# Kernel optimization log

Measured on AMD Instinct MI355X. Metric: run time of the kernel, lower is better.

## Reference

```python
import jax, jax.numpy as jnp
import numpy as np
from jax import lax

B, N, HID = 2, 1024, 2048
H, D, HKV = 32, 64, 8
GROUPS = H // HKV
CHUNK = 64
MAG = 0.5
GATE_NORM = 16.0


def setup_inputs() -> dict:
    key = jax.random.key(0)
    ks = jax.random.split(key, 5)
    hidden_states = jax.random.normal(ks[0], (B, N, HID), jnp.float32)
    Wq = jax.random.normal(ks[1], (HID, H * D), jnp.float32) * 0.02
    Wk = jax.random.normal(ks[2], (HID, HKV * D), jnp.float32) * 0.02
    Wv = jax.random.normal(ks[3], (HID, HKV * D), jnp.float32) * 0.02
    Wo = jax.random.normal(ks[4], (H * D, HID), jnp.float32) * 0.02
    return {"hidden_states": hidden_states, "Wq": Wq, "Wk": Wk, "Wv": Wv, "Wo": Wo}


def _repeat_kv(x, g):
    # [b, hkv, n, d] -> [b, hkv*g, n, d]
    return jnp.repeat(x, g, axis=1)


def _delta_rule_chunked(q, k, v, beta, chunk):
    """Chunked delta-rule linear attention (DeltaNet-style) with elementwise beta gate."""
    b, h, n, d = q.shape
    nc = n // chunk
    qc, kc, vc, bc = (x.reshape(b, h, nc, chunk, d) for x in (q, k, v, beta))
    k_beta = kc * bc
    v_beta = vc * bc
    # T = (I + tril(k_beta k^T, -1))^{-1}, a unit lower-triangular solve per chunk
    strict = jnp.tril(jnp.ones((chunk, chunk), bool), -1)
    L = jnp.einsum('bhnid,bhnjd->bhnij', k_beta, kc) * strict
    M = L + jnp.eye(chunk, dtype=q.dtype)
    eye = jnp.broadcast_to(jnp.eye(chunk, dtype=q.dtype), M.shape)
    T = jax.scipy.linalg.solve_triangular(M, eye, lower=True, unit_diagonal=True)
    u = jnp.einsum('bhnij,bhnjd->bhnid', T, v_beta)   # pseudo-values
    w = jnp.einsum('bhnij,bhnjd->bhnid', T, k_beta)   # pseudo-keys
    causal = jnp.tril(jnp.ones((chunk, chunk), bool))

    def step(S, xs):
        qi, ki, ui, wi = xs  # each [b, h, chunk, d]; S: [b, h, d, d]
        u_p = ui - jnp.einsum('bhcd,bhde->bhce', wi, S)
        attn = jnp.einsum('bhid,bhjd->bhij', qi, ki) * causal
        o = jnp.einsum('bhcd,bhde->bhce', qi, S) + jnp.einsum('bhij,bhjd->bhid', attn, u_p)
        S_new = S + jnp.einsum('bhcd,bhce->bhde', ki, u_p)
        return S_new, o

    xs = tuple(jnp.moveaxis(x, 2, 0) for x in (qc, kc, u, w))  # [nc, b, h, chunk, d]
    S0 = jnp.zeros((b, h, d, d), q.dtype)
    S_final, o = lax.scan(step, S0, xs)
    o = jnp.moveaxis(o, 0, 2).reshape(b, h, n, d)
    return o, S_final


def reference(hidden_states, Wq, Wk, Wv, Wo):
    b, n, _ = hidden_states.shape
    q = hidden_states @ Wq            # [b, n, H*D]
    k = hidden_states @ Wk            # [b, n, HKV*D]
    v = hidden_states @ Wv            # [b, n, HKV*D]
    g = k  # AdaptiveAvgPool1d(512 -> 512) is the identity here

    qh = q.reshape(b, n, H, D).transpose(0, 2, 1, 3)      # [b, H, n, D]
    kh = k.reshape(b, n, HKV, D).transpose(0, 2, 1, 3)    # [b, HKV, n, D]
    vh = v.reshape(b, n, HKV, D).transpose(0, 2, 1, 3)
    gh = g.reshape(b, n, HKV, D).transpose(0, 2, 1, 3)
    k_rep = _repeat_kv(kh, GROUPS)
    v_rep = _repeat_kv(vh, GROUPS)
    g_rep = _repeat_kv(gh, GROUPS)

    # linear-attention branch: softmax feature maps + log-sigmoid gate
    ql = jax.nn.softmax(qh, axis=-1).astype(jnp.float32)
    kl = jax.nn.softmax(k_rep, axis=-1).astype(jnp.float32)
    gl = (jax.nn.log_sigmoid(g_rep) / GATE_NORM).astype(jnp.float32)
    o_lin, _ = _delta_rule_chunked(ql, kl, v_rep.astype(jnp.float32), gl, CHUNK)
    o_lin = o_lin.transpose(0, 2, 1, 3).reshape(b, n, H * D) @ Wo

    # base (vanilla causal) attention branch
    scale = 1.0 / np.sqrt(D).astype(np.float32)
    scores = jnp.einsum('bhid,bhjd->bhij', qh, k_rep) * scale
    causal = jnp.tril(jnp.ones((n, n), bool))
    scores = jnp.where(causal, scores, jnp.finfo(scores.dtype).min)
    attn_weights = jax.nn.softmax(scores, axis=-1)
    o_base = jnp.einsum('bhij,bhjd->bhid', attn_weights, v_rep)
    o_base = o_base.transpose(0, 2, 1, 3).reshape(b, n, H * D) @ Wo

    out = MAG * o_lin + (1.0 - MAG) * o_base
    return out, attn_weights
```

## Files before the change

kernel.cpp:

```cpp
#include <hip/hip_runtime.h>
#include <hip/hip_bf16.h>

constexpr int Bc = 2, Nc = 1024, HIDc = 2048, Hc = 32, Dc = 64, HKVc = 8, NCc = 16;

typedef unsigned short bfu;
typedef __attribute__((ext_vector_type(8))) short frag_ab;
typedef __attribute__((ext_vector_type(4))) float frag_cd;

__device__ __forceinline__ bfu f2bf(float f) {
  unsigned int u = __float_as_uint(f);
  unsigned int r = u + 0x7fffu + ((u >> 16) & 1u);
  return (bfu)(r >> 16);
}
__device__ __forceinline__ ushort4 pack4(float4 v) {
  ushort4 r; r.x = f2bf(v.x); r.y = f2bf(v.y); r.z = f2bf(v.z); r.w = f2bf(v.w);
  return r;
}

__device__ __forceinline__ void gl16(const bfu* g, bfu* l) {
  __builtin_amdgcn_global_load_lds(
      (const __attribute__((address_space(1))) void*)g,
      (__attribute__((address_space(3))) void*)l, 16, 0, 0);
}

__global__ __launch_bounds__(256) void cast_bf16_k(
    const float* __restrict__ in, bfu* __restrict__ out)
{
  const size_t i = ((size_t)blockIdx.x * 256 + threadIdx.x) * 4;
  *(ushort4*)(out + i) = pack4(*(const float4*)(in + i));
}

__global__ __launch_bounds__(256) void transpose_cast_k(
    const float* __restrict__ W, bfu* __restrict__ WT, int K, int N)
{
  __shared__ float t[32][33];
  const int bn = blockIdx.x * 32, bk = blockIdx.y * 32;
  const int x = threadIdx.x & 31, y = threadIdx.x >> 5;
#pragma unroll
  for (int i = 0; i < 32; i += 8)
    t[y + i][x] = W[(size_t)(bk + y + i) * N + bn + x];
  __syncthreads();
#pragma unroll
  for (int i = 0; i < 32; i += 8)
    WT[(size_t)(bn + y + i) * K + bk + x] = f2bf(t[x][y + i]);
}

__global__ __launch_bounds__(256) void transpose_v_k(
    const float* __restrict__ v, bfu* __restrict__ vt)
{
  __shared__ __align__(16) bfu T[64][72];
  const int blk = blockIdx.x;
  const int nt = blk & 15, bh = blk >> 4;
  const int hk = bh & 7, b = bh >> 3;
  const int tid = threadIdx.x;
  const int n = tid >> 2, dv0 = (tid & 3) * 16;
  const float* src = v + ((size_t)(b * Nc + nt * 64 + n) * 8 + hk) * 64 + dv0;
#pragma unroll
  for (int e = 0; e < 16; ++e) T[dv0 + e][n] = f2bf(src[e]);
  __syncthreads();
  const int r = tid >> 3, c = (tid & 7) * 8;
#pragma unroll
  for (int hh = 0; hh < 2; ++hh) {
    const int dv = r + hh * 32;
    *(uint4*)(vt + ((size_t)(bh * 64 + dv)) * 1024 + nt * 64 + c) =
        *(const uint4*)&T[dv][c];
  }
}

__device__ __forceinline__ void gemm128_gl(
    const bfu* __restrict__ A, const bfu* __restrict__ BT,
    float* __restrict__ C, const int Nn, const int m0, const int n0,
    bfu* As, bfu* Bs)
{
  const int tid = threadIdx.x;
  const int wave = tid >> 6, lane = tid & 63;
  const int wm = (wave >> 1) * 64, wn = (wave & 1) * 64;
  const int fm = lane & 15, quad = lane >> 4;
  const int sr = tid >> 2, skc = (tid & 3) * 8;

  frag_cd acc[4][4];
#pragma unroll
  for (int i = 0; i < 4; ++i)
#pragma unroll
    for (int j = 0; j < 4; ++j) acc[i][j] = (frag_cd){0.f, 0.f, 0.f, 0.f};

  const bfu* Ag = A + (size_t)(m0 + sr) * 2048 + skc;
  const bfu* Bg = BT + (size_t)(n0 + sr) * 2048 + skc;
  bfu* Al = As + tid * 8;
  bfu* Bl = Bs + tid * 8;

  for (int k0 = 0; k0 < 2048; k0 += 32) {
    gl16(Ag + k0, Al);
    gl16(Ag + k0 + (size_t)64 * 2048, Al + 64 * 32);
    gl16(Bg + k0, Bl);
    gl16(Bg + k0 + (size_t)64 * 2048, Bl + 64 * 32);
    __syncthreads();
    frag_ab a[4], b[4];
#pragma unroll
    for (int im = 0; im < 4; ++im)
      a[im] = *(const frag_ab*)&As[(size_t)(wm + im * 16 + fm) * 32 + quad * 8];
#pragma unroll
    for (int in = 0; in < 4; ++in)
      b[in] = *(const frag_ab*)&Bs[(size_t)(wn + in * 16 + fm) * 32 + quad * 8];
#pragma unroll
    for (int im = 0; im < 4; ++im)
#pragma unroll
      for (int in = 0; in < 4; ++in)
        acc[im][in] = __builtin_amdgcn_mfma_f32_16x16x32_bf16(
            a[im], b[in], acc[im][in], 0, 0, 0);
    __syncthreads();
  }
#pragma unroll
  for (int im = 0; im < 4; ++im)
#pragma unroll
    for (int in = 0; in < 4; ++in) {
      const int n = n0 + wn + in * 16 + fm;
#pragma unroll
      for (int r = 0; r < 4; ++r) {
        const int m = m0 + wm + im * 16 + quad * 4 + r;
        C[(size_t)m * Nn + n] = acc[im][in][r];
      }
    }
}

__global__ __launch_bounds__(256) void gemm_qkv_k(
    const bfu* __restrict__ A, const bfu* __restrict__ BTq,
    const bfu* __restrict__ BTk, const bfu* __restrict__ BTv,
    float* __restrict__ Cq, float* __restrict__ Ck, float* __restrict__ Cv)
{
  __shared__ __align__(16) bfu As[128 * 32];
  __shared__ __align__(16) bfu Bs[128 * 32];
  int bx = blockIdx.x;
  const bfu* BT; float* C; int Nn;
  if (bx < 16)      { BT = BTq; C = Cq; Nn = 2048; }
  else if (bx < 20) { BT = BTk; C = Ck; Nn = 512; bx -= 16; }
  else              { BT = BTv; C = Cv; Nn = 512; bx -= 20; }
  gemm128_gl(A, BT, C, Nn, blockIdx.y * 128, bx * 128, As, Bs);
}

__global__ __launch_bounds__(256) void gemm_wo_k(
    const bfu* __restrict__ A, const bfu* __restrict__ BT, float* __restrict__ C)
{
  __shared__ __align__(16) bfu As[128 * 32];
  __shared__ __align__(16) bfu Bs[128 * 32];
  gemm128_gl(A, BT, C, 2048, blockIdx.y * 128, blockIdx.x * 128, As, Bs);
}

__global__ __launch_bounds__(256) void gates64_k(
    const float* __restrict__ kin, float* __restrict__ kl, float* __restrict__ gl,
    bfu* __restrict__ k_bf)
{
  const int r = blockIdx.x * 4 + (threadIdx.x >> 6);
  const int lane = threadIdx.x & 63;
  const size_t idx = (size_t)r * 64 + lane;
  const float x = kin[idx];
  k_bf[idx] = f2bf(x);
  float m = x;
#pragma unroll
  for (int o = 32; o > 0; o >>= 1) m = fmaxf(m, __shfl_xor(m, o, 64));
  const float e = __expf(x - m);
  float s = e;
#pragma unroll
  for (int o = 32; o > 0; o >>= 1) s += __shfl_xor(s, o, 64);
  kl[idx] = e / s;
  const float ls = fminf(x, 0.f) - log1pf(__expf(-fabsf(x)));
  gl[idx] = ls * 0.0625f;
}

__global__ __launch_bounds__(256) void chunk_prep_k(
    const float* __restrict__ kl, const float* __restrict__ v,
    const float* __restrict__ gl, float* __restrict__ u_out, float* __restrict__ w_out)
{
  __shared__ __align__(16) float KC[64][68];
  __shared__ float KB[64][65];
  __shared__ float VB[64][65];
  const int blk = blockIdx.x;
  const int c = blk & 15, bh = blk >> 4;
  const int hk = bh & 7, b = bh >> 3;
  const int tid = threadIdx.x;
  for (int x = tid; x < 4096; x += 256) {
    const int i = x >> 6, d = x & 63;
    const size_t src = ((size_t)(b * Nc + c * 64 + i) * 8 + hk) * 64 + d;
    const float kv = kl[src], g = gl[src], vv = v[src];
    KC[d][i] = kv; KB[i][d] = kv * g; VB[i][d] = vv * g;
  }
  __syncthreads();
  const int li = tid >> 2, j0 = (tid & 3) * 16;
  float acc[16];
#pragma unroll
  for (int jj = 0; jj < 16; ++jj) acc[jj] = 0.f;
  for (int d = 0; d < 64; ++d) {
    const float kb = KB[li][d];
    const float4 c0v = *(const float4*)&KC[d][j0];
    const float4 c1v = *(const float4*)&KC[d][j0 + 4];
    const float4 c2v = *(const float4*)&KC[d][j0 + 8];
    const float4 c3v = *(const float4*)&KC[d][j0 + 12];
    acc[0] += kb * c0v.x;  acc[1] += kb * c0v.y;  acc[2] += kb * c0v.z;  acc[3] += kb * c0v.w;
    acc[4] += kb * c1v.x;  acc[5] += kb * c1v.y;  acc[6] += kb * c1v.z;  acc[7] += kb * c1v.w;
    acc[8] += kb * c2v.x;  acc[9] += kb * c2v.y;  acc[10] += kb * c2v.z; acc[11] += kb * c2v.w;
    acc[12] += kb * c3v.x; acc[13] += kb * c3v.y; acc[14] += kb * c3v.z; acc[15] += kb * c3v.w;
  }
  __syncthreads();
#pragma unroll
  for (int jj = 0; jj < 16; ++jj)
    KC[li][j0 + jj] = (j0 + jj < li) ? acc[jj] : 0.f;
  __syncthreads();
  for (int r0 = 0; r0 < 64; r0 += 16) {
    if (r0 > 0) {
      for (int p = tid; p < 2048; p += 256) {
        const int ii = p >> 7, dc = p & 127;
        float (*X)[65] = (dc < 64) ? VB : KB;
        const int d = dc & 63;
        float a2 = X[r0 + ii][d];
        for (int j = 0; j < r0; ++j) a2 -= KC[r0 + ii][j] * X[j][d];
        X[r0 + ii][d] = a2;
      }
      __syncthreads();
    }
    if (tid < 128) {
      const int d = tid & 63;
      float (*X)[65] = (tid < 64) ? VB : KB;
      for (int i = r0 + 1; i < r0 + 16; ++i) {
        float a2 = X[i][d];
        for (int j = r0; j < i; ++j) a2 -= KC[i][j] * X[j][d];
        X[i][d] = a2;
      }
    }
    __syncthreads();
  }
  for (int x = tid; x < 4096; x += 256) {
    u_out[(size_t)blk * 4096 + x] = VB[x >> 6][x & 63];
    w_out[(size_t)blk * 4096 + x] = KB[x >> 6][x & 63];
  }
}

__global__ __launch_bounds__(256) void scan_k(
    const float* __restrict__ u_ps, const float* __restrict__ w_ps,
    const float* __restrict__ kl, float* __restrict__ u_p, float* __restrict__ S_pre)
{
  __shared__ __align__(16) float S[64][20];
  __shared__ __align__(16) float up[64][20];
  __shared__ __align__(16) float kw[64][68];
  __shared__ __align__(16) float kt[64][68];
  const int blk = blockIdx.x;
  const int cg = blk & 3;
  const int bh = blk >> 2;
  const int hk = bh & 7, b = bh >> 3;
  const int t = threadIdx.x;
  const int row = t >> 2;
  const int c0 = (t & 3) * 4;
  const int cbase = cg * 16;
  for (int x = t; x < 1024; x += 256) S[x >> 4][x & 15] = 0.f;
  __syncthreads();
  for (int c = 0; c < 16; ++c) {
    const size_t cb = ((size_t)bh * 16 + c) * 4096;
    const float4 upre = *(const float4*)(u_ps + cb + row * 64 + cbase + c0);
    for (int x = t; x < 1024; x += 256) {
      const int i = x >> 4, d4 = (x & 15) * 4;
      *(float4*)&kw[i][d4] = *(const float4*)(w_ps + cb + i * 64 + d4);
      *(float4*)&kt[i][d4] =
          *(const float4*)(kl + ((size_t)(b * Nc + c * 64 + i) * 8 + hk) * 64 + d4);
    }
    for (int x = t; x < 1024; x += 256) {
      const int i = x >> 4, cc = x & 15;
      S_pre[cb + i * 64 + cbase + cc] = S[i][cc];
    }
    __syncthreads();
    {
      float a0 = upre.x, a1 = upre.y, a2 = upre.z, a3 = upre.w;
      for (int e4 = 0; e4 < 64; e4 += 4) {
        const float4 wv4 = *(const float4*)&kw[row][e4];
#pragma unroll
        for (int ee = 0; ee < 4; ++ee) {
          const float wv = ((const float*)&wv4)[ee];
          const float4 sv = *(const float4*)&S[e4 + ee][c0];
          a0 -= wv * sv.x; a1 -= wv * sv.y; a2 -= wv * sv.z; a3 -= wv * sv.w;
        }
      }
      const float4 o = make_float4(a0, a1, a2, a3);
      *(float4*)&up[row][c0] = o;
      *(float4*)(u_p + cb + row * 64 + cbase + c0) = o;
    }
    __syncthreads();
    {
      const float4 sv = *(const float4*)&S[row][c0];
      float s0 = sv.x, s1 = sv.y, s2 = sv.z, s3 = sv.w;
      for (int i = 0; i < 64; ++i) {
        const float kv = kt[i][row];
        const float4 uv = *(const float4*)&up[i][c0];
        s0 += kv * uv.x; s1 += kv * uv.y; s2 += kv * uv.z; s3 += kv * uv.w;
      }
      *(float4*)&S[row][c0] = make_float4(s0, s1, s2, s3);
    }
    __syncthreads();
  }
}

__global__ __launch_bounds__(256) void olin_k(
    const float* __restrict__ qraw, const float* __restrict__ kl,
    const float* __restrict__ upb, const float* __restrict__ S_pre,
    float* __restrict__ o_comb)
{
  __shared__ float Q[64][65];
  __shared__ __align__(16) float Bb[64][68];
  __shared__ float At[64][65];
  const int blk = blockIdx.x;
  const int c = blk & 15, bh = blk >> 4;
  const int h = bh & 31, b = bh >> 5, hk = h >> 2;
  const int tid = threadIdx.x;
  const int i = tid >> 2, d0 = (tid & 3) * 16;
  for (int x = tid; x < 4096; x += 256) {
    const int r = x >> 6, d = x & 63;
    Q[r][d] = qraw[((size_t)(b * Nc + c * 64 + r) * 32 + h) * 64 + d];
    Bb[d][r] = kl[((size_t)(b * Nc + c * 64 + r) * 8 + hk) * 64 + d];
  }
  __syncthreads();
  {
    float mx = -1e30f;
#pragma unroll
    for (int j = 0; j < 16; ++j) mx = fmaxf(mx, Q[i][d0 + j]);
#pragma unroll
    for (int o = 1; o < 4; o <<= 1) mx = fmaxf(mx, __shfl_xor(mx, o, 64));
    float ev[16];
    float sum = 0.f;
#pragma unroll
    for (int j = 0; j < 16; ++j) { ev[j] = __expf(Q[i][d0 + j] - mx); sum += ev[j]; }
#pragma unroll
    for (int o = 1; o < 4; o <<= 1) sum += __shfl_xor(sum, o, 64);
    const float inv = 1.f / sum;
#pragma unroll
    for (int j = 0; j < 16; ++j) Q[i][d0 + j] = ev[j] * inv;
  }
  __syncthreads();
  {
    float a[16];
#pragma unroll
    for (int j = 0; j < 16; ++j) a[j] = 0.f;
    for (int d = 0; d < 64; ++d) {
      const float qv = Q[i][d];
      const float4 b0 = *(const float4*)&Bb[d][d0];
      const float4 b1 = *(const float4*)&Bb[d][d0 + 4];
      const float4 b2 = *(const float4*)&Bb[d][d0 + 8];
      const float4 b3 = *(const float4*)&Bb[d][d0 + 12];
      a[0] += qv * b0.x;  a[1] += qv * b0.y;  a[2] += qv * b0.z;  a[3] += qv * b0.w;
      a[4] += qv * b1.x;  a[5] += qv * b1.y;  a[6] += qv * b1.z;  a[7] += qv * b1.w;
      a[8] += qv * b2.x;  a[9] += qv * b2.y;  a[10] += qv * b2.z; a[11] += qv * b2.w;
      a[12] += qv * b3.x; a[13] += qv * b3.y; a[14] += qv * b3.z; a[15] += qv * b3.w;
    }
#pragma unroll
    for (int j = 0; j < 16; ++j) At[i][d0 + j] = (d0 + j <= i) ? a[j] : 0.f;
  }
  __syncthreads();
  const size_t cb = ((size_t)(b * 8 + hk) * 16 + c) * 4096;
  for (int x = tid; x < 4096; x += 256) Bb[x >> 6][x & 63] = S_pre[cb + x];
  __syncthreads();
  float o[16];
#pragma unroll
  for (int j = 0; j < 16; ++j) o[j] = 0.f;
  for (int e = 0; e < 64; ++e) {
    const float qv = Q[i][e];
#pragma unroll
    for (int j = 0; j < 16; ++j) o[j] += qv * Bb[e][d0 + j];
  }
  __syncthreads();
  for (int x = tid; x < 4096; x += 256) Bb[x >> 6][x & 63] = upb[cb + x];
  __syncthreads();
  for (int j2 = 0; j2 < 64; ++j2) {
    const float av = At[i][j2];
#pragma unroll
    for (int j = 0; j < 16; ++j) o[j] += av * Bb[j2][d0 + j];
  }
  float* oc = o_comb + ((size_t)(b * Nc + c * 64 + i) * 32 + h) * 64 + d0;
#pragma unroll
  for (int j = 0; j < 16; ++j) oc[j] = 0.5f * o[j];
}

template <int LDK>
__device__ __forceinline__ void stage_tile(
    const bfu* __restrict__ g, size_t row_stride, bfu* dst, int tid)
{
  const int xr = tid >> 3;
  const int xc = (tid & 7) * 8;
#pragma unroll
  for (int hh = 0; hh < 2; ++hh) {
    const int row = xr + hh * 32;
    *(uint4*)&dst[(size_t)row * LDK + xc] =
        *(const uint4*)(g + (size_t)row * row_stride + xc);
  }
}

__global__ __launch_bounds__(256) void ml_mfma_k(
    const bfu* __restrict__ qbf, const bfu* __restrict__ kbf,
    float* __restrict__ mbuf, float* __restrict__ lbuf)
{
  constexpr int LDK = 72;
  __shared__ __align__(16) bfu Qt[64 * LDK];
  __shared__ __align__(16) bfu Kt[64 * LDK];
  __shared__ float mred[4][64];
  __shared__ float lred[4][64];
  const int blk = blockIdx.x;
  const int ib = blk & 15, bh = blk >> 4;
  const int h = bh & 31, b = bh >> 5, hk = h >> 2;
  const int tid = threadIdx.x;
  const int wave = tid >> 6, lane = tid & 63;
  const int fm = lane & 15, quad = lane >> 4;
  const int wj = wave * 16;

  stage_tile<LDK>(qbf + ((size_t)(b * Nc + ib * 64) * 32 + h) * 64,
                  (size_t)32 * 64, Qt, tid);
  __syncthreads();
  frag_ab qb[4][2];
#pragma unroll
  for (int in = 0; in < 4; ++in)
#pragma unroll
    for (int kk = 0; kk < 2; ++kk)
      qb[in][kk] = *(const frag_ab*)&Qt[(size_t)(in * 16 + fm) * LDK + kk * 32 + quad * 8];

  float m[4], l[4];
#pragma unroll
  for (int in = 0; in < 4; ++in) { m[in] = -1e30f; l[in] = 0.f; }

  for (int jt = 0; jt <= ib; ++jt) {
    __syncthreads();
    stage_tile<LDK>(kbf + ((size_t)(b * Nc + jt * 64) * 8 + hk) * 64,
                    (size_t)8 * 64, Kt, tid);
    __syncthreads();
    frag_ab ka[2];
    ka[0] = *(const frag_ab*)&Kt[(size_t)(wj + fm) * LDK + quad * 8];
    ka[1] = *(const frag_ab*)&Kt[(size_t)(wj + fm) * LDK + 32 + quad * 8];
    const bool diag = (jt == ib);
#pragma unroll
    for (int in = 0; in < 4; ++in) {
      frag_cd acc = (frag_cd){0.f, 0.f, 0.f, 0.f};
      acc = __builtin_amdgcn_mfma_f32_16x16x32_bf16(ka[0], qb[in][0], acc, 0, 0, 0);
      acc = __builtin_amdgcn_mfma_f32_16x16x32_bf16(ka[1], qb[in][1], acc, 0, 0, 0);
      const int iloc = in * 16 + fm;
      float sv[4];
      bool vd[4];
      float tm = -1e30f;
#pragma unroll
      for (int r = 0; r < 4; ++r) {
        const int jloc = wj + quad * 4 + r;
        vd[r] = !diag || (jloc <= iloc);
        sv[r] = acc[r] * 0.125f;
        if (vd[r]) tm = fmaxf(tm, sv[r]);
      }
      const float mn = fmaxf(m[in], tm);
      float lsum = 0.f;
#pragma unroll
      for (int r = 0; r < 4; ++r)
        if (vd[r]) lsum += __expf(sv[r] - mn);
      l[in] = l[in] * __expf(m[in] - mn) + lsum;
      m[in] = mn;
    }
  }
#pragma unroll
  for (int in = 0; in < 4; ++in) {
    float mm = m[in], ll = l[in];
#pragma unroll
    for (int off = 16; off < 64; off <<= 1) {
      const float mo = __shfl_xor(mm, off, 64);
      const float lo = __shfl_xor(ll, off, 64);
      const float mn = fmaxf(mm, mo);
      ll = ll * __expf(mm - mn) + lo * __expf(mo - mn);
      mm = mn;
    }
    if (quad == 0) { mred[wave][in * 16 + fm] = mm; lred[wave][in * 16 + fm] = ll; }
  }
  __syncthreads();
  if (tid < 64) {
    float M = -1e30f;
#pragma unroll
    for (int w = 0; w < 4; ++w) M = fmaxf(M, mred[w][tid]);
    float L = 0.f;
#pragma unroll
    for (int w = 0; w < 4; ++w) L += lred[w][tid] * __expf(mred[w][tid] - M);
    const size_t rowi = (size_t)(b * 32 + h) * 1024 + ib * 64 + tid;
    mbuf[rowi] = M;
    lbuf[rowi] = L;
  }
}

__global__ __launch_bounds__(256) void pv_mfma_k(
    const bfu* __restrict__ qbf, const bfu* __restrict__ kbf,
    const bfu* __restrict__ vtbf, const float* __restrict__ mbuf,
    const float* __restrict__ lbuf, float* __restrict__ attn,
    const float* __restrict__ o_comb, bfu* __restrict__ oc_bf)
{
  constexpr int LDK = 72;
  __shared__ __align__(16) bfu Qt[64 * LDK];
  __shared__ __align__(16) bfu Kt[64 * LDK];
  __shared__ __align__(16) bfu Vt[64 * LDK];
  __shared__ __align__(16) bfu Pmat[64 * LDK];
  const int blk = blockIdx.x;
  const int ib = blk & 15, bh = blk >> 4;
  const int h = bh & 31, b = bh >> 5, hk = h >> 2;
  const int tid = threadIdx.x;
  const int wave = tid >> 6, lane = tid & 63;
  const int fm = lane & 15, quad = lane >> 4;
  const int wj = wave * 16;
  const int im0 = wave * 16;

  stage_tile<LDK>(qbf + ((size_t)(b * Nc + ib * 64) * 32 + h) * 64,
                  (size_t)32 * 64, Qt, tid);
  __syncthreads();
  frag_ab qb[4][2];
#pragma unroll
  for (int in = 0; in < 4; ++in)
#pragma unroll
    for (int kk = 0; kk < 2; ++kk)
      qb[in][kk] = *(const frag_ab*)&Qt[(size_t)(in * 16 + fm) * LDK + kk * 32 + quad * 8];

  float mi[4], il[4];
#pragma unroll
  for (int in = 0; in < 4; ++in) {
    const size_t rowi = (size_t)(b * 32 + h) * 1024 + ib * 64 + in * 16 + fm;
    mi[in] = mbuf[rowi];
    il[in] = 1.f / lbuf[rowi];
  }

  float* arow0 = attn + ((size_t)(b * 32 + h) * 1024 + ib * 64) * 1024;

  frag_cd o[4];
#pragma unroll
  for (int in = 0; in < 4; ++in) o[in] = (frag_cd){0.f, 0.f, 0.f, 0.f};

  for (int jt = 0; jt <= ib; ++jt) {
    __syncthreads();
    stage_tile<LDK>(kbf + ((size_t)(b * Nc + jt * 64) * 8 + hk) * 64,
                    (size_t)8 * 64, Kt, tid);
    stage_tile<LDK>(vtbf + (size_t)(b * 8 + hk) * 64 * 1024 + jt * 64,
                    (size_t)1024, Vt, tid);
    __syncthreads();
    frag_ab ka[2];
    ka[0] = *(const frag_ab*)&Kt[(size_t)(wj + fm) * LDK + quad * 8];
    ka[1] = *(const frag_ab*)&Kt[(size_t)(wj + fm) * LDK + 32 + quad * 8];
    const bool diag = (jt == ib);
#pragma unroll
    for (int in = 0; in < 4; ++in) {
      frag_cd acc = (frag_cd){0.f, 0.f, 0.f, 0.f};
      acc = __builtin_amdgcn_mfma_f32_16x16x32_bf16(ka[0], qb[in][0], acc, 0, 0, 0);
      acc = __builtin_amdgcn_mfma_f32_16x16x32_bf16(ka[1], qb[in][1], acc, 0, 0, 0);
      const int iloc = in * 16 + fm;
      float p[4];
#pragma unroll
      for (int r = 0; r < 4; ++r) {
        const int jloc = wj + quad * 4 + r;
        const bool vdr = !diag || (jloc <= iloc);
        p[r] = vdr ? __expf(acc[r] * 0.125f - mi[in]) * il[in] : 0.f;
      }
      *(float4*)(arow0 + (size_t)iloc * 1024 + jt * 64 + wj + quad * 4) =
          make_float4(p[0], p[1], p[2], p[3]);
      ushort4 w;
      w.x = f2bf(p[0]); w.y = f2bf(p[1]); w.z = f2bf(p[2]); w.w = f2bf(p[3]);
      *(ushort4*)&Pmat[(size_t)iloc * LDK + wj + quad * 4] = w;
    }
    __syncthreads();
    frag_ab pa[2];
    pa[0] = *(const frag_ab*)&Pmat[(size_t)(im0 + fm) * LDK + quad * 8];
    pa[1] = *(const frag_ab*)&Pmat[(size_t)(im0 + fm) * LDK + 32 + quad * 8];
#pragma unroll
    for (int in = 0; in < 4; ++in) {
      frag_ab vb0 = *(const frag_ab*)&Vt[(size_t)(in * 16 + fm) * LDK + quad * 8];
      frag_ab vb1 = *(const frag_ab*)&Vt[(size_t)(in * 16 + fm) * LDK + 32 + quad * 8];
      o[in] = __builtin_amdgcn_mfma_f32_16x16x32_bf16(pa[0], vb0, o[in], 0, 0, 0);
      o[in] = __builtin_amdgcn_mfma_f32_16x16x32_bf16(pa[1], vb1, o[in], 0, 0, 0);
    }
  }
  for (int jt2 = ib + 1; jt2 < 16; ++jt2) {
    const float4 z = make_float4(0.f, 0.f, 0.f, 0.f);
    for (int x = tid; x < 1024; x += 256) {
      const int row = x >> 4, c4 = (x & 15) * 4;
      *(float4*)(arow0 + (size_t)row * 1024 + jt2 * 64 + c4) = z;
    }
  }
#pragma unroll
  for (int in = 0; in < 4; ++in)
#pragma unroll
    for (int r = 0; r < 4; ++r) {
      const int i = im0 + quad * 4 + r;
      const size_t idx = ((size_t)(b * Nc + ib * 64 + i) * 32 + h) * 64 + in * 16 + fm;
      oc_bf[idx] = f2bf(o_comb[idx] + 0.5f * o[in][r]);
    }
}

extern "C" void kernel_launch(void* const* d_in, const int* in_sizes, int n_in,
                              void* d_out, int out_size, void* d_ws, size_t ws_size,
                              hipStream_t stream) {
  const float* hs = (const float*)d_in[0];
  const float* Wq = (const float*)d_in[1];
  const float* Wk = (const float*)d_in[2];
  const float* Wv = (const float*)d_in[3];
  const float* Wo = (const float*)d_in[4];
  float* out = (float*)d_out;
  float* attn = out + (size_t)Bc * Nc * HIDc;

  float* ws = (float*)d_ws;
  float* q_raw  = ws;
  float* k_raw  = q_raw + 4194304;
  float* v_raw  = k_raw + 1048576;
  float* kl     = v_raw + 1048576;
  float* gl     = kl + 1048576;
  float* u_ps   = gl + 1048576;
  float* w_ps   = u_ps + 2097152;
  float* upb    = w_ps + 2097152;
  float* S_pre  = upb + 2097152;
  float* o_comb = S_pre + 2097152;
  float* mbuf   = o_comb + 4194304;
  float* lbuf   = mbuf + 65536;
  bfu* bstart = (bfu*)(lbuf + 65536);
  bfu* hs_bf  = bstart;
  bfu* WqT    = hs_bf + 4194304;
  bfu* WkT    = WqT + 4194304;
  bfu* WvT    = WkT + 1048576;
  bfu* WoT    = WvT + 1048576;
  bfu* oc_bf  = WoT + 4194304;
  bfu* q_bf   = hs_bf;
  bfu* k_bf   = WqT;
  bfu* vt_bf  = WqT + 1048576;

  cast_bf16_k<<<4096, 256, 0, stream>>>(hs, hs_bf);
  transpose_cast_k<<<dim3(64, 64), 256, 0, stream>>>(Wq, WqT, 2048, 2048);
  transpose_cast_k<<<dim3(16, 64), 256, 0, stream>>>(Wk, WkT, 2048, 512);
  transpose_cast_k<<<dim3(16, 64), 256, 0, stream>>>(Wv, WvT, 2048, 512);
  transpose_cast_k<<<dim3(64, 64), 256, 0, stream>>>(Wo, WoT, 2048, 2048);
  gemm_qkv_k<<<dim3(24, 16), 256, 0, stream>>>(hs_bf, WqT, WkT, WvT,
                                               q_raw, k_raw, v_raw);
  cast_bf16_k<<<4096, 256, 0, stream>>>(q_raw, q_bf);
  gates64_k<<<4096, 256, 0, stream>>>(k_raw, kl, gl, k_bf);
  transpose_v_k<<<256, 256, 0, stream>>>(v_raw, vt_bf);
  chunk_prep_k<<<256, 256, 0, stream>>>(kl, v_raw, gl, u_ps, w_ps);
  scan_k<<<64, 256, 0, stream>>>(u_ps, w_ps, kl, upb, S_pre);
  olin_k<<<1024, 256, 0, stream>>>(q_raw, kl, upb, S_pre, o_comb);
  ml_mfma_k<<<1024, 256, 0, stream>>>(q_bf, k_bf, mbuf, lbuf);
  pv_mfma_k<<<1024, 256, 0, stream>>>(q_bf, k_bf, vt_bf, mbuf, lbuf, attn,
                                      o_comb, oc_bf);
  gemm_wo_k<<<dim3(16, 16), 256, 0, stream>>>(oc_bf, WoT, out);
}
```

Baseline: 676.7 us.

## Fuse softmax stats and PV kernels; cast q to bf16 inside olin

The row max/sum pass and the P·V/attention-write pass are merged into one kernel. The per-row statistics now stay in shared memory instead of going through global mbuf/lbuf, and the Q tile load is done once. The separate q→bf16 cast kernel is dropped, with olin_k writing the bf16 copy while it loads q. olin_k's inner accumulation loops also read shared memory as float4. This cuts two launches and some global traffic, at the cost of higher LDS use per block in the fused kernel, which may lower occupancy.

```diff
diff --git a/kernel.cpp b/kernel.cpp
--- a/kernel.cpp
+++ b/kernel.cpp
@@ -299,7 +299,7 @@
 __global__ __launch_bounds__(256) void olin_k(
     const float* __restrict__ qraw, const float* __restrict__ kl,
     const float* __restrict__ upb, const float* __restrict__ S_pre,
-    float* __restrict__ o_comb)
+    float* __restrict__ o_comb, bfu* __restrict__ q_bf)
 {
   __shared__ float Q[64][65];
   __shared__ __align__(16) float Bb[64][68];
@@ -311,7 +311,10 @@
   const int i = tid >> 2, d0 = (tid & 3) * 16;
   for (int x = tid; x < 4096; x += 256) {
     const int r = x >> 6, d = x & 63;
-    Q[r][d] = qraw[((size_t)(b * Nc + c * 64 + r) * 32 + h) * 64 + d];
+    const size_t qidx = ((size_t)(b * Nc + c * 64 + r) * 32 + h) * 64 + d;
+    const float qv = qraw[qidx];
+    Q[r][d] = qv;
+    q_bf[qidx] = f2bf(qv);
     Bb[d][r] = kl[((size_t)(b * Nc + c * 64 + r) * 8 + hk) * 64 + d];
   }
   __syncthreads();
@@ -359,16 +362,28 @@
   for (int j = 0; j < 16; ++j) o[j] = 0.f;
   for (int e = 0; e < 64; ++e) {
     const float qv = Q[i][e];
-#pragma unroll
-    for (int j = 0; j < 16; ++j) o[j] += qv * Bb[e][d0 + j];
+    const float4 b0 = *(const float4*)&Bb[e][d0];
+    const float4 b1 = *(const float4*)&Bb[e][d0 + 4];
+    const float4 b2 = *(const float4*)&Bb[e][d0 + 8];
+    const float4 b3 = *(const float4*)&Bb[e][d0 + 12];
+    o[0] += qv * b0.x;  o[1] += qv * b0.y;  o[2] += qv * b0.z;  o[3] += qv * b0.w;
+    o[4] += qv * b1.x;  o[5] += qv * b1.y;  o[6] += qv * b1.z;  o[7] += qv * b1.w;
+    o[8] += qv * b2.x;  o[9] += qv * b2.y;  o[10] += qv * b2.z; o[11] += qv * b2.w;
+    o[12] += qv * b3.x; o[13] += qv * b3.y; o[14] += qv * b3.z; o[15] += qv * b3.w;
   }
   __syncthreads();
   for (int x = tid; x < 4096; x += 256) Bb[x >> 6][x & 63] = upb[cb + x];
   __syncthreads();
   for (int j2 = 0; j2 < 64; ++j2) {
     const float av = At[i][j2];
-#pragma unroll
-    for (int j = 0; j < 16; ++j) o[j] += av * Bb[j2][d0 + j];
+    const float4 b0 = *(const float4*)&Bb[j2][d0];
+    const float4 b1 = *(const float4*)&Bb[j2][d0 + 4];
+    const float4 b2 = *(const float4*)&Bb[j2][d0 + 8];
+    const float4 b3 = *(const float4*)&Bb[j2][d0 + 12];
+    o[0] += av * b0.x;  o[1] += av * b0.y;  o[2] += av * b0.z;  o[3] += av * b0.w;
+    o[4] += av * b1.x;  o[5] += av * b1.y;  o[6] += av * b1.z;  o[7] += av * b1.w;
+    o[8] += av * b2.x;  o[9] += av * b2.y;  o[10] += av * b2.z; o[11] += av * b2.w;
+    o[12] += av * b3.x; o[13] += av * b3.y; o[14] += av * b3.z; o[15] += av * b3.w;
   }
   float* oc = o_comb + ((size_t)(b * Nc + c * 64 + i) * 32 + h) * 64 + d0;
 #pragma unroll
@@ -389,15 +404,20 @@
   }
 }
 
-__global__ __launch_bounds__(256) void ml_mfma_k(
+__global__ __launch_bounds__(256) void attn_mfma_k(
     const bfu* __restrict__ qbf, const bfu* __restrict__ kbf,
-    float* __restrict__ mbuf, float* __restrict__ lbuf)
+    const bfu* __restrict__ vtbf, float* __restrict__ attn,
+    const float* __restrict__ o_comb, bfu* __restrict__ oc_bf)
 {
   constexpr int LDK = 72;
   __shared__ __align__(16) bfu Qt[64 * LDK];
   __shared__ __align__(16) bfu Kt[64 * LDK];
+  __shared__ __align__(16) bfu Vt[64 * LDK];
+  __shared__ __align__(16) bfu Pmat[64 * LDK];
   __shared__ float mred[4][64];
   __shared__ float lred[4][64];
+  __shared__ float mfin[64];
+  __shared__ float lfin[64];
   const int blk = blockIdx.x;
   const int ib = blk & 15, bh = blk >> 4;
   const int h = bh & 31, b = bh >> 5, hk = h >> 2;
@@ -405,6 +425,7 @@
   const int wave = tid >> 6, lane = tid & 63;
   const int fm = lane & 15, quad = lane >> 4;
   const int wj = wave * 16;
+  const int im0 = wave * 16;
 
   stage_tile<LDK>(qbf + ((size_t)(b * Nc + ib * 64) * 32 + h) * 64,
                   (size_t)32 * 64, Qt, tid);
@@ -475,52 +496,18 @@
     float L = 0.f;
 #pragma unroll
     for (int w = 0; w < 4; ++w) L += lred[w][tid] * __expf(mred[w][tid] - M);
-    const size_t rowi = (size_t)(b * 32 + h) * 1024 + ib * 64 + tid;
-    mbuf[rowi] = M;
-    lbuf[rowi] = L;
-  }
-}
-
-__global__ __launch_bounds__(256) void pv_mfma_k(
-    const bfu* __restrict__ qbf, const bfu* __restrict__ kbf,
-    const bfu* __restrict__ vtbf, const float* __restrict__ mbuf,
-    const float* __restrict__ lbuf, float* __restrict__ attn,
-    const float* __restrict__ o_comb, bfu* __restrict__ oc_bf)
-{
-  constexpr int LDK = 72;
-  __shared__ __align__(16) bfu Qt[64 * LDK];
-  __shared__ __align__(16) bfu Kt[64 * LDK];
-  __shared__ __align__(16) bfu Vt[64 * LDK];
-  __shared__ __align__(16) bfu Pmat[64 * LDK];
-  const int blk = blockIdx.x;
-  const int ib = blk & 15, bh = blk >> 4;
-  const int h = bh & 31, b = bh >> 5, hk = h >> 2;
-  const int tid = threadIdx.x;
-  const int wave = tid >> 6, lane = tid & 63;
-  const int fm = lane & 15, quad = lane >> 4;
-  const int wj = wave * 16;
-  const int im0 = wave * 16;
-
-  stage_tile<LDK>(qbf + ((size_t)(b * Nc + ib * 64) * 32 + h) * 64,
-                  (size_t)32 * 64, Qt, tid);
-  __syncthreads();
-  frag_ab qb[4][2];
-#pragma unroll
-  for (int in = 0; in < 4; ++in)
-#pragma unroll
-    for (int kk = 0; kk < 2; ++kk)
-      qb[in][kk] = *(const frag_ab*)&Qt[(size_t)(in * 16 + fm) * LDK + kk * 32 + quad * 8];
-
+    mfin[tid] = M;
+    lfin[tid] = L;
+  }
+  __syncthreads();
   float mi[4], il[4];
 #pragma unroll
   for (int in = 0; in < 4; ++in) {
-    const size_t rowi = (size_t)(b * 32 + h) * 1024 + ib * 64 + in * 16 + fm;
-    mi[in] = mbuf[rowi];
-    il[in] = 1.f / lbuf[rowi];
+    mi[in] = mfin[in * 16 + fm];
+    il[in] = 1.f / lfin[in * 16 + fm];
   }
 
   float* arow0 = attn + ((size_t)(b * 32 + h) * 1024 + ib * 64) * 1024;
-
   frag_cd o[4];
 #pragma unroll
   for (int in = 0; in < 4; ++in) o[in] = (frag_cd){0.f, 0.f, 0.f, 0.f};
@@ -626,14 +613,11 @@
   transpose_cast_k<<<dim3(64, 64), 256, 0, stream>>>(Wo, WoT, 2048, 2048);
   gemm_qkv_k<<<dim3(24, 16), 256, 0, stream>>>(hs_bf, WqT, WkT, WvT,
                                                q_raw, k_raw, v_raw);
-  cast_bf16_k<<<4096, 256, 0, stream>>>(q_raw, q_bf);
   gates64_k<<<4096, 256, 0, stream>>>(k_raw, kl, gl, k_bf);
   transpose_v_k<<<256, 256, 0, stream>>>(v_raw, vt_bf);
   chunk_prep_k<<<256, 256, 0, stream>>>(kl, v_raw, gl, u_ps, w_ps);
   scan_k<<<64, 256, 0, stream>>>(u_ps, w_ps, kl, upb, S_pre);
-  olin_k<<<1024, 256, 0, stream>>>(q_raw, kl, upb, S_pre, o_comb);
-  ml_mfma_k<<<1024, 256, 0, stream>>>(q_bf, k_bf, mbuf, lbuf);
-  pv_mfma_k<<<1024, 256, 0, stream>>>(q_bf, k_bf, vt_bf, mbuf, lbuf, attn,
-                                      o_comb, oc_bf);
+  olin_k<<<1024, 256, 0, stream>>>(q_raw, kl, upb, S_pre, o_comb, q_bf);
+  attn_mfma_k<<<1024, 256, 0, stream>>>(q_bf, k_bf, vt_bf, attn, o_comb, oc_bf);
   gemm_wo_k<<<dim3(16, 16), 256, 0, stream>>>(oc_bf, WoT, out);
 }
```

After: 650.9 us. 1.04x faster.
